# Performance work log

Hardware: AMD Instinct MI355X
Metric: run time of the kernel (lower is better)

Reference implementation:

```python
import jax, jax.numpy as jnp
import numpy as np

NUM_SAMPLE = 10   # self._num, hard-coded as range(10) in prob_sample
FSCALE = 5        # neighbor-count kernel
CSCALE = 3        # constraint-count kernel
EPS = 1e-16


def _sum_window(x, k):
    # x: [N,H,W] -> SAME-padded k x k box sum == F.conv2d with ones(1,1,k,k), padding=(k-1)//2
    return jax.lax.reduce_window(x, 0.0, jax.lax.add, (1, k, k), (1, 1, 1), 'SAME')


def _dilate8(x):
    # 3x3 max-pool = one step of 8-connectivity dilation (skimage flood_fill default
    # connectivity for 2D is full connectivity when my_connectivity is None)
    return jax.lax.reduce_window(x, 0.0, jax.lax.max, (1, 3, 3), (1, 1, 1), 'SAME')


def _flood_fill(fg, seed_r, seed_c):
    # fg: [N,H,W] binary float; returns the fg-connected component containing the seed,
    # via fixed-point iteration of masked dilation (equivalent to skimage.flood_fill
    # seeded at the max-neighbor pixel, then thresholding the filled value).
    N, H, W = fg.shape
    reach0 = jnp.zeros_like(fg).at[jnp.arange(N), seed_r, seed_c].set(1.0) * fg

    def cond(st):
        _, changed, it = st
        return changed & (it < H * W)

    def body(st):
        reach, _, it = st
        new = jnp.maximum(reach, _dilate8(reach) * fg)
        return new, jnp.any(new > reach), it + 1

    reach, _, _ = jax.lax.while_loop(cond, body, (reach0, jnp.array(True), jnp.int32(0)))
    return reach


def connectivity_rewards(sample_ns, fg_num):
    # sample_ns: [n, S, H, W] int class indices. Returns binary rewards [n, S, H, W]
    # (reward_type='binary', run_state='train'). All (image, sample) pairs processed
    # in one batched flood fill per foreground class.
    n, S, H, W = sample_ns.shape
    flat = sample_ns.reshape(n * S, H, W)
    total = jnp.zeros((n * S, H, W), jnp.float32)
    for class_idx in range(1, fg_num):  # small fixed loop over fg classes
        fg = (flat == class_idx).astype(jnp.float32)
        neigh = _sum_window(fg, FSCALE) * fg           # count_neighbor * fg
        neigh_flat = neigh.reshape(n * S, H * W)
        seed = jnp.argmax(neigh_flat, axis=-1)          # pixel with max neighbor count
        has_fg = (jnp.max(neigh_flat, axis=-1) > 0).astype(jnp.float32)
        fill = _flood_fill(fg, seed // W, seed % W) * has_fg[:, None, None]
        Fc = _sum_window(fill, CSCALE) * fill           # F_fg_neigbors
        Sc = _sum_window(fg, CSCALE) * fg               # S_fg_neigbors
        r = (jnp.where(Fc == 0, -1.0, Fc) == jnp.where(Sc == 0, -2.0, Sc)).astype(jnp.float32)
        total = total + r
    return total.reshape(n, S, H, W)


def setup_inputs() -> dict:
    key = jax.random.key(0)
    logits = jax.random.normal(key, (4, 4, 512, 512), dtype=jnp.float32)
    preds = jax.nn.softmax(logits, axis=1)  # per-pixel class probabilities [n,c,h,w]
    return {"preds": preds}


def reference(preds):
    n, c, h, w = preds.shape
    skey = jax.random.key(42)
    # prob_sample: per-pixel multinomial over classes, repeated NUM_SAMPLE times
    lg = jnp.moveaxis(jnp.log(preds + EPS), 1, -1)  # [n,h,w,c]
    samp = jax.random.categorical(skey, lg, axis=-1, shape=(NUM_SAMPLE, n, h, w))
    sample_ns = jnp.transpose(samp, (1, 0, 2, 3)).astype(jnp.int32)  # [n,S,h,w]
    prob_ns = jnp.take_along_axis(preds, sample_ns, axis=1)          # [n,S,h,w]
    rewards = jax.lax.stop_gradient(connectivity_rewards(sample_ns, c))
    # REINFORCE objective: maximize reward-weighted log-prob of sampled labelings
    loss = -(rewards * jnp.log(prob_ns + EPS)).mean()
    return loss
```

## Files before the change

kernel.cpp:

```cpp
#include <hip/hip_runtime.h>
#include <stdint.h>

#define SNUM 10
#define NBATCH 4
#define NCLS 4
#define HH 512
#define WW 512
#define IMG (HH*WW)
#define NPIX (SNUM*NBATCH*IMG)
#define WPI (IMG/32)
#define QCAP 3584

#define SCRATCH_OFF (4096 + NPIX/4)

__device__ __forceinline__ float u01(uint32_t bits) {
  const float f = __uint_as_float((bits >> 9) | 0x3f800000u) - 1.0f;
  return fmaxf(f, 1.17549435e-38f);
}

__device__ __forceinline__ uint32_t unpack32(uint64_t v) {
  uint64_t tt = v | (v >> 1);
  uint64_t u = ~tt & 0x5555555555555555ULL;
  u = (u ^ (u >> 1))  & 0x3333333333333333ULL;
  u = (u ^ (u >> 2))  & 0x0F0F0F0F0F0F0F0FULL;
  u = (u ^ (u >> 4))  & 0x00FF00FF00FF00FFULL;
  u = (u ^ (u >> 8))  & 0x0000FFFF0000FFFFULL;
  u = (u ^ (u >> 16)) & 0x00000000FFFFFFFFULL;
  return (uint32_t)u;
}

__global__ __launch_bounds__(256) void k_sample(const float* __restrict__ preds,
                                                uint8_t* __restrict__ packed,
                                                float* __restrict__ acc,
                                                uint32_t* __restrict__ gkey,
                                                uint32_t* __restrict__ misc) {
  const int t = blockIdx.x * 256 + threadIdx.x;
  if (t == 0) acc[0] = 0.0f;
  if (t < 120) gkey[t] = 0u;
  if (t >= 120 && t < 256) misc[t - 120] = 0u;
  const int sn = t >> 16;
  const int n  = sn & 3;
  const int pg = t & 65535;
  const int pix = pg << 2;

  float pp[NCLS][4];
#pragma unroll
  for (int c = 0; c < NCLS; ++c) {
    const float4 v = *reinterpret_cast<const float4*>(
        preds + (((int64_t)(n * NCLS + c)) << 18) + pix);
    pp[c][0] = v.x; pp[c][1] = v.y; pp[c][2] = v.z; pp[c][3] = v.w;
  }

  const uint32_t gb = (uint32_t)sn * 1048576u + ((uint32_t)pix << 2);
  const uint32_t k1 = 42u;
  const uint32_t k2 = 42u ^ 0x1BD11BDAu;
  uint32_t byte = 0;

#define TFR4(r) { \
  _Pragma("unroll") \
  for (int c_ = 0; c_ < 4; ++c_) { \
    x0[c_] += x1[c_]; \
    const uint32_t xr_ = x1[c_]; \
    x1[c_] = ((xr_ << (r)) | (xr_ >> (32 - (r)))) ^ x0[c_]; \
  } }
#define INJ4(a, b) { \
  _Pragma("unroll") \
  for (int c_ = 0; c_ < 4; ++c_) { x0[c_] += (a); x1[c_] += (b); } }

#pragma unroll
  for (int j = 0; j < 4; ++j) {
    uint32_t x0[4], x1[4];
#pragma unroll
    for (int c = 0; c < 4; ++c) {
      x0[c] = 0u;
      x1[c] = gb + (uint32_t)(4 * j + c) + k1;
    }
    TFR4(13) TFR4(15) TFR4(26) TFR4(6)
    INJ4(k1, k2 + 1u)
    TFR4(17) TFR4(29) TFR4(16) TFR4(24)
    INJ4(k2, 2u)
    TFR4(13) TFR4(15) TFR4(26) TFR4(6)
    INJ4(0u, k1 + 3u)
    TFR4(17) TFR4(29) TFR4(16) TFR4(24)
    INJ4(k1, k2 + 4u)
    TFR4(13) TFR4(15) TFR4(26) TFR4(6)
    float lg[4];
#pragma unroll
    for (int c = 0; c < 4; ++c)
      lg[c] = __log2f(u01((x0[c] + k2) ^ (x1[c] + 5u)));

    float bp = pp[0][j];
    float bl = lg[0];
    int bc = 0;
#pragma unroll
    for (int c = 1; c < NCLS; ++c) {
      if (pp[c][j] * bl < bp * lg[c]) { bp = pp[c][j]; bl = lg[c]; bc = c; }
    }
    byte |= (uint32_t)bc << (2 * j);
  }
#undef TFR4
#undef INJ4
  packed[t] = (uint8_t)byte;
}


__device__ __forceinline__ uint32_t runmask(uint32_t m, uint32_t s) {
  uint32_t out = 0;
  while (s) {
    const int j = __ffs(s) - 1;
    const uint32_t bj = 1u << j;
    const uint32_t up = ((m + bj) ^ m) & m;
    const uint32_t rm = __brev(m);
    const uint32_t rbj = 1u << (31 - j);
    const uint32_t dn = __brev(((rm + rbj) ^ rm) & rm);
    const uint32_t run = up | dn;
    out |= run;
    s &= ~run;
  }
  return out;
}

__device__ __forceinline__ void claimf(uint32_t* fg, uint32_t* qw, uint32_t* qb,
                                       uint32_t* qtail, uint32_t t, uint32_t want) {
  const uint32_t old = atomicAnd(&fg[t], ~want);
  uint32_t nb = old & want;
  if (!nb) return;
  const uint32_t ext = runmask(old, nb) & ~nb;
  if (ext) {
    const uint32_t old2 = atomicAnd(&fg[t], ~ext);
    nb |= old2 & ext;
  }
  const uint32_t slot = atomicAdd(qtail, 1u);
  if (slot < QCAP) { atomicExch(&qw[slot], t); atomicExch(&qb[slot], nb); }
}

__device__ __forceinline__ uint64_t shup64(uint64_t v) {
  const uint32_t lo = __shfl_up((unsigned int)v, 1, 64);
  const uint32_t hi = __shfl_up((unsigned int)(v >> 32), 1, 64);
  return ((uint64_t)hi << 32) | lo;
}
__device__ __forceinline__ uint64_t shdn64(uint64_t v) {
  const uint32_t lo = __shfl_down((unsigned int)v, 1, 64);
  const uint32_t hi = __shfl_down((unsigned int)(v >> 32), 1, 64);
  return ((uint64_t)hi << 32) | lo;
}

__global__ __launch_bounds__(256) void k_af(const float* __restrict__ preds,
                                            const uint8_t* __restrict__ packed,
                                            uint32_t* __restrict__ gkey,
                                            uint32_t* __restrict__ misc,
                                            float* __restrict__ acc,
                                            float* __restrict__ out,
                                            uint32_t* __restrict__ scratch) {
  __shared__ uint32_t sfg[36 * 16];
  __shared__ uint32_t skey;
  __shared__ uint32_t sfin;
  __shared__ uint32_t sbk;
  __shared__ uint32_t sfb;
  __shared__ uint32_t stail;
  __shared__ float    sred[4];
  const int tid = threadIdx.x;
  const int b = blockIdx.x;
  const int prob = b >> 4;
  const int slab = b & 15;
  const int sn = prob % 40;
  const int k  = 1 + prob / 40;
  const int n  = sn & 3;
  if (tid == 0) skey = 0u;

  const uint64_t* p64 = reinterpret_cast<const uint64_t*>(packed);
  const uint64_t pat = (uint64_t)k * 0x5555555555555555ULL;

  const int gr0 = slab * 32 - 2;
  for (int wi = tid; wi < 36 * 16; wi += 256) {
    const int gr = gr0 + (wi >> 4);
    uint32_t m = 0;
    if (gr >= 0 && gr < HH)
      m = unpack32(p64[(int64_t)sn * WPI + (gr << 4) + (wi & 15)] ^ pat);
    sfg[wi] = m;
  }
  __syncthreads();

  uint32_t lbest = 0;
  for (int idx = tid; idx < 512; idx += 256) {
    const int rl = 2 + (idx >> 4);
    const int col = idx & 15;
    const uint32_t cw = sfg[(rl << 4) + col];
    if (!cw) continue;
    uint64_t rb[5];
#pragma unroll
    for (int d = 0; d < 5; ++d) {
      const int base = ((rl + d - 2) << 4) + col;
      const uint32_t le = (col > 0)  ? sfg[base - 1] : 0u;
      const uint32_t cu = sfg[base];
      const uint32_t ri = (col < 15) ? sfg[base + 1] : 0u;
      rb[d] = ((uint64_t)(ri & 7u) << 34) | ((uint64_t)cu << 2) | (uint64_t)(le >> 30);
    }
    const int gr = slab * 32 + (idx >> 4);
    uint32_t bits = cw;
    while (bits) {
      const int j = __ffs(bits) - 1;
      bits &= bits - 1;
      int cnt = 0;
#pragma unroll
      for (int d = 0; d < 5; ++d)
        cnt += __popc((uint32_t)(rb[d] >> j) & 0x1fu);
      const uint32_t fidx = (uint32_t)((gr << 9) + (col << 5) + j);
      const uint32_t key = ((uint32_t)cnt << 18) | (0x3FFFFu - fidx);
      lbest = lbest > key ? lbest : key;
    }
  }
#pragma unroll
  for (int off = 32; off > 0; off >>= 1) {
    const uint32_t o = (uint32_t)__shfl_down((int)lbest, off, 64);
    lbest = lbest > o ? lbest : o;
  }
  if ((tid & 63) == 0 && lbest) atomicMax(&skey, lbest);
  __syncthreads();

  if (tid == 0) {
    if (skey) atomicMax(&gkey[prob], skey);
    __threadfence();
    const uint32_t a = atomicAdd(&misc[8 + prob], 1u);
    uint32_t f = 0u;
    if (a == 15u) { f = 1u; sbk = atomicAdd(&gkey[prob], 0u); }
    sfin = f;
    sfb = 0u;
  }
  __syncthreads();
  if (!sfin) return;

  uint32_t* qtail = scratch;
  uint32_t* fgg   = scratch + 16;
  uint32_t* qw    = scratch + 16 + WPI;
  uint32_t* qb    = scratch + 16 + WPI + QCAP;
  const uint32_t bkey = sbk;
  const uint32_t seed = 0x3FFFFu - (bkey & 0x3FFFFu);
  const float* chan = preds + (((int64_t)n) * NCLS + k) * (int64_t)IMG;
  float local = 0.0f;

  if ((bkey >> 18) != 0u) {
    if (tid < 64) {
      const int sr = (int)(seed >> 9), sc = (int)(seed & 511);
      int r0 = sr - 31; if (r0 < 0) r0 = 0; if (r0 > HH - 64) r0 = HH - 64;
      int cl = (sc >> 5) - (((sc & 31) < 16) ? 1 : 0);
      if (cl < 0) cl = 0; if (cl > 14) cl = 14;
      const int ar = r0 + tid;
      const int64_t pb = (int64_t)sn * WPI + (ar << 4) + cl;
      const uint64_t fgw = ((uint64_t)unpack32(p64[pb + 1] ^ pat) << 32)
                         |            unpack32(p64[pb]     ^ pat);
      const uint64_t rfg = __brevll(fgw);
      uint64_t fill = (ar == sr) ? (1ULL << (sc - (cl << 5))) : 0ULL;

      bool conv = false;
      for (int it = 0; it < 2048; ++it) {
        uint64_t up = shup64(fill); if (tid == 0)  up = 0ULL;
        uint64_t dn = shdn64(fill); if (tid == 63) dn = 0ULL;
        const uint64_t sp = fill | up | dn;
        uint64_t s = fgw & (sp | (sp << 1) | (sp >> 1));
        uint64_t nf = 0ULL;
        while (s) {
          const int j = __ffsll((unsigned long long)s) - 1;
          const uint64_t upr = ((fgw + (1ULL << j)) ^ fgw) & fgw;
          const uint64_t dnr = __brevll(((rfg + (1ULL << (63 - j))) ^ rfg) & rfg);
          const uint64_t run = upr | dnr;
          nf |= run;
          s &= ~run;
        }
        const bool ch = (nf != fill);
        fill = nf;
        if (__ballot(ch) == 0ULL) { conv = true; break; }
      }

      bool esc = !conv;
      if (fill) {
        if (tid == 0 && r0 > 0) esc = true;
        if (tid == 63 && r0 + 63 < HH - 1) esc = true;
        if ((fill & 1ULL) && cl > 0) esc = true;
        if ((fill >> 63) && cl < 14) esc = true;
      }

      if (__ballot(esc) == 0ULL) {
        uint64_t bits = fill;
        const float* rowp = chan + (int64_t)ar * WW + (cl << 5);
        while (bits) {
          const int j = __ffsll((unsigned long long)bits) - 1;
          bits &= bits - 1;
          local += logf(rowp[j] + 1e-16f);
        }
      } else if (tid == 0) {
        sfb = 1u;
      }
    }
    __syncthreads();

    if (sfb) {
      if (tid == 0) {
        const uint32_t tk = atomicAdd(&misc[1], 1u);
        while (atomicAdd(&misc[2], 0u) != tk) __builtin_amdgcn_s_sleep(32);
        atomicExch(qtail, 0u);
      }
      __syncthreads();
      for (int wi = tid; wi < WPI; wi += 256)
        atomicExch(&fgg[wi], unpack32(p64[(int64_t)sn * WPI + wi] ^ pat));
      __syncthreads();
      claimf(fgg, qw, qb, qtail, seed >> 5, 1u << (seed & 31));
      uint32_t head = 0;
      while (true) {
        __syncthreads();
        if (tid == 0) { uint32_t tl = atomicAdd(qtail, 0u); stail = tl > QCAP ? QCAP : tl; }
        __syncthreads();
        const uint32_t tail = stail;
        if (head >= tail) break;
        for (uint32_t i = head + (uint32_t)tid; i < tail; i += 256) {
          const uint32_t w = atomicAdd(&qw[i], 0u), got = atomicAdd(&qb[i], 0u);
          const int row = (int)(w >> 4), cb = (int)(w & 15);
          const uint32_t spread = got | (got << 1) | (got >> 1);
          const bool lo = (got & 1u) != 0u, hi = (got >> 31) != 0u;
          if (row > 0) {
            claimf(fgg, qw, qb, qtail, w - 16, spread);
            if (cb > 0 && lo)  claimf(fgg, qw, qb, qtail, w - 17, 0x80000000u);
            if (cb < 15 && hi) claimf(fgg, qw, qb, qtail, w - 15, 1u);
          }
          if (row < HH - 1) {
            claimf(fgg, qw, qb, qtail, w + 16, spread);
            if (cb > 0 && lo)  claimf(fgg, qw, qb, qtail, w + 15, 0x80000000u);
            if (cb < 15 && hi) claimf(fgg, qw, qb, qtail, w + 17, 1u);
          }
          if (cb > 0 && lo)  claimf(fgg, qw, qb, qtail, w - 1, 0x80000000u);
          if (cb < 15 && hi) claimf(fgg, qw, qb, qtail, w + 1, 1u);
        }
        head = tail;
      }
      const uint32_t tot = stail;
      for (uint32_t i = (uint32_t)tid; i < tot; i += 256) {
        const uint32_t w = atomicAdd(&qw[i], 0u);
        uint32_t bits = atomicAdd(&qb[i], 0u);
        const int row = (int)(w >> 4);
        const int colb = (int)(w & 15) << 5;
        const float* rowp = chan + (int64_t)row * WW;
        while (bits) {
          const int j = __ffs(bits) - 1;
          bits &= bits - 1;
          local += logf(rowp[colb + j] + 1e-16f);
        }
      }
      __syncthreads();
      if (tid == 0) atomicAdd(&misc[2], 1u);
    }
  }

#pragma unroll
  for (int off = 32; off > 0; off >>= 1)
    local += __shfl_down(local, off, 64);
  if ((tid & 63) == 0) sred[tid >> 6] = local;
  __syncthreads();
  if (tid == 0) {
    const float tot = sred[0] + sred[1] + sred[2] + sred[3];
    if (tot != 0.0f) atomicAdd(acc, tot);
    __threadfence();
    const uint32_t old = atomicAdd(&misc[0], 1u);
    if (old == 119u) {
      const float s = atomicAdd(acc, 0.0f);
      out[0] = -s / 10485760.0f;
    }
  }
}

extern "C" void kernel_launch(void* const* d_in, const int* in_sizes, int n_in,
                              void* d_out, int out_size, void* d_ws, size_t ws_size,
                              hipStream_t stream) {
  const float* preds = (const float*)d_in[0];
  float* out = (float*)d_out;
  char* ws = (char*)d_ws;
  float*    acc     = (float*)ws;
  uint32_t* gkey    = (uint32_t*)(ws + 64);
  uint32_t* misc    = (uint32_t*)(ws + 1536);
  uint8_t*  packed  = (uint8_t*)(ws + 4096);
  uint32_t* scratch = (uint32_t*)(ws + SCRATCH_OFF);

  k_sample<<<10240, 256, 0, stream>>>(preds, packed, acc, gkey, misc);
  k_af<<<1920, 256, 0, stream>>>(preds, packed, gkey, misc, acc, out, scratch);
}
```

Before: 180.4 us.

## Move fallback flood-fill queue and mask into per-block LDS, drop global lock

The rare fallback flood fill now keeps the foreground bitmap and BFS queue in shared memory per block instead of a global scratch buffer. This removes the global ticket lock that serialized fallback blocks and the global atomics on the queue. In exchange, each block reserves about 61 KB of LDS, which limits k_af to roughly one resident block per CU, including the common early-exit path.

```diff
diff --git a/kernel.cpp b/kernel.cpp
--- a/kernel.cpp
+++ b/kernel.cpp
@@ -11,7 +11,6 @@
 #define WPI (IMG/32)
 #define QCAP 3584
 
-#define SCRATCH_OFF (4096 + NPIX/4)
 
 __device__ __forceinline__ float u01(uint32_t bits) {
   const float f = __uint_as_float((bits >> 9) | 0x3f800000u) - 1.0f;
@@ -131,7 +130,7 @@
     nb |= old2 & ext;
   }
   const uint32_t slot = atomicAdd(qtail, 1u);
-  if (slot < QCAP) { atomicExch(&qw[slot], t); atomicExch(&qb[slot], nb); }
+  if (slot < QCAP) { qw[slot] = t; qb[slot] = nb; }
 }
 
 __device__ __forceinline__ uint64_t shup64(uint64_t v) {
@@ -150,9 +149,9 @@
                                             uint32_t* __restrict__ gkey,
                                             uint32_t* __restrict__ misc,
                                             float* __restrict__ acc,
-                                            float* __restrict__ out,
-                                            uint32_t* __restrict__ scratch) {
-  __shared__ uint32_t sfg[36 * 16];
+                                            float* __restrict__ out) {
+  __shared__ uint32_t lds[WPI + 2 * QCAP];
+  __shared__ uint32_t qtail;
   __shared__ uint32_t skey;
   __shared__ uint32_t sfin;
   __shared__ uint32_t sbk;
@@ -170,6 +169,7 @@
 
   const uint64_t* p64 = reinterpret_cast<const uint64_t*>(packed);
   const uint64_t pat = (uint64_t)k * 0x5555555555555555ULL;
+  uint32_t* sfg = lds;
 
   const int gr0 = slab * 32 - 2;
   for (int wi = tid; wi < 36 * 16; wi += 256) {
@@ -230,10 +230,6 @@
   __syncthreads();
   if (!sfin) return;
 
-  uint32_t* qtail = scratch;
-  uint32_t* fgg   = scratch + 16;
-  uint32_t* qw    = scratch + 16 + WPI;
-  uint32_t* qb    = scratch + 16 + WPI + QCAP;
   const uint32_t bkey = sbk;
   const uint32_t seed = 0x3FFFFu - (bkey & 0x3FFFFu);
   const float* chan = preds + (((int64_t)n) * NCLS + k) * (int64_t)IMG;
@@ -295,47 +291,45 @@
     __syncthreads();
 
     if (sfb) {
-      if (tid == 0) {
-        const uint32_t tk = atomicAdd(&misc[1], 1u);
-        while (atomicAdd(&misc[2], 0u) != tk) __builtin_amdgcn_s_sleep(32);
-        atomicExch(qtail, 0u);
-      }
+      uint32_t* fgb = lds;
+      uint32_t* qw  = lds + WPI;
+      uint32_t* qb  = lds + WPI + QCAP;
+      if (tid == 0) qtail = 0u;
+      for (int wi = tid; wi < WPI; wi += 256)
+        fgb[wi] = unpack32(p64[(int64_t)sn * WPI + wi] ^ pat);
       __syncthreads();
-      for (int wi = tid; wi < WPI; wi += 256)
-        atomicExch(&fgg[wi], unpack32(p64[(int64_t)sn * WPI + wi] ^ pat));
-      __syncthreads();
-      claimf(fgg, qw, qb, qtail, seed >> 5, 1u << (seed & 31));
+      claimf(fgb, qw, qb, &qtail, seed >> 5, 1u << (seed & 31));
       uint32_t head = 0;
       while (true) {
         __syncthreads();
-        if (tid == 0) { uint32_t tl = atomicAdd(qtail, 0u); stail = tl > QCAP ? QCAP : tl; }
+        if (tid == 0) { uint32_t tl = qtail; stail = tl > QCAP ? QCAP : tl; }
         __syncthreads();
         const uint32_t tail = stail;
         if (head >= tail) break;
         for (uint32_t i = head + (uint32_t)tid; i < tail; i += 256) {
-          const uint32_t w = atomicAdd(&qw[i], 0u), got = atomicAdd(&qb[i], 0u);
+          const uint32_t w = qw[i], got = qb[i];
           const int row = (int)(w >> 4), cb = (int)(w & 15);
           const uint32_t spread = got | (got << 1) | (got >> 1);
           const bool lo = (got & 1u) != 0u, hi = (got >> 31) != 0u;
           if (row > 0) {
-            claimf(fgg, qw, qb, qtail, w - 16, spread);
-            if (cb > 0 && lo)  claimf(fgg, qw, qb, qtail, w - 17, 0x80000000u);
-            if (cb < 15 && hi) claimf(fgg, qw, qb, qtail, w - 15, 1u);
+            claimf(fgb, qw, qb, &qtail, w - 16, spread);
+            if (cb > 0 && lo)  claimf(fgb, qw, qb, &qtail, w - 17, 0x80000000u);
+            if (cb < 15 && hi) claimf(fgb, qw, qb, &qtail, w - 15, 1u);
           }
           if (row < HH - 1) {
-            claimf(fgg, qw, qb, qtail, w + 16, spread);
-            if (cb > 0 && lo)  claimf(fgg, qw, qb, qtail, w + 15, 0x80000000u);
-            if (cb < 15 && hi) claimf(fgg, qw, qb, qtail, w + 17, 1u);
+            claimf(fgb, qw, qb, &qtail, w + 16, spread);
+            if (cb > 0 && lo)  claimf(fgb, qw, qb, &qtail, w + 15, 0x80000000u);
+            if (cb < 15 && hi) claimf(fgb, qw, qb, &qtail, w + 17, 1u);
           }
-          if (cb > 0 && lo)  claimf(fgg, qw, qb, qtail, w - 1, 0x80000000u);
-          if (cb < 15 && hi) claimf(fgg, qw, qb, qtail, w + 1, 1u);
+          if (cb > 0 && lo)  claimf(fgb, qw, qb, &qtail, w - 1, 0x80000000u);
+          if (cb < 15 && hi) claimf(fgb, qw, qb, &qtail, w + 1, 1u);
         }
         head = tail;
       }
       const uint32_t tot = stail;
       for (uint32_t i = (uint32_t)tid; i < tot; i += 256) {
-        const uint32_t w = atomicAdd(&qw[i], 0u);
-        uint32_t bits = atomicAdd(&qb[i], 0u);
+        const uint32_t w = qw[i];
+        uint32_t bits = qb[i];
         const int row = (int)(w >> 4);
         const int colb = (int)(w & 15) << 5;
         const float* rowp = chan + (int64_t)row * WW;
@@ -345,8 +339,6 @@
           local += logf(rowp[colb + j] + 1e-16f);
         }
       }
-      __syncthreads();
-      if (tid == 0) atomicAdd(&misc[2], 1u);
     }
   }
 
@@ -373,12 +365,11 @@
   const float* preds = (const float*)d_in[0];
   float* out = (float*)d_out;
   char* ws = (char*)d_ws;
-  float*    acc     = (float*)ws;
-  uint32_t* gkey    = (uint32_t*)(ws + 64);
-  uint32_t* misc    = (uint32_t*)(ws + 1536);
-  uint8_t*  packed  = (uint8_t*)(ws + 4096);
-  uint32_t* scratch = (uint32_t*)(ws + SCRATCH_OFF);
+  float*    acc    = (float*)ws;
+  uint32_t* gkey   = (uint32_t*)(ws + 64);
+  uint32_t* misc   = (uint32_t*)(ws + 1536);
+  uint8_t*  packed = (uint8_t*)(ws + 4096);
 
   k_sample<<<10240, 256, 0, stream>>>(preds, packed, acc, gkey, misc);
-  k_af<<<1920, 256, 0, stream>>>(preds, packed, gkey, misc, acc, out, scratch);
-}
+  k_af<<<1920, 256, 0, stream>>>(preds, packed, gkey, misc, acc, out);
+}
```

Result: slower. 194.3 us (+7.7%).
